# Optimization experiments

Measured on AMD Instinct MI355X. Metric: run time of the kernel, lower is better.

Reference implementation:

```python
import jax, jax.numpy as jnp
import numpy as np

B, T, H, N = 2, 1024, 32, 64
HN = H * N              # 2048 hidden size
KVH, KVD = 8, 512       # GQA kv heads / kv width; repeat = HN // KVD = 4
LW, LA, LV, LG, LK = 64, 64, 32, 128, 32   # wavgk_split_list
EPS = 1e-6

def _rms(x, w):
    xf = x.astype(jnp.float32)
    var = jnp.mean(xf * xf, axis=-1, keepdims=True)
    return (w * (xf * jax.lax.rsqrt(var + EPS))).astype(x.dtype)

def _rot_half(x):
    x1, x2 = jnp.split(x, 2, axis=-1)
    return jnp.concatenate([-x2, x1], axis=-1)

def setup_inputs():
    key = jax.random.key(0)
    ks = iter(jax.random.split(key, 32))
    nrm = lambda s, sc=1.0: jax.random.normal(next(ks), s, jnp.float32) * sc
    d = {
        'x_in': nrm((B, T, HN)),
        'v_first': nrm((B, T, KVH, N)),
        'k_first': nrm((B, T, KVH, N)),
        'state': jnp.zeros((B, H, N, N), jnp.float32),
    }
    pos = jnp.arange(T, dtype=jnp.float32)
    inv = 1.0 / (10000.0 ** (jnp.arange(0, N, 2, dtype=jnp.float32) / N))
    ang = pos[:, None] * inv[None, :]
    ang = jnp.concatenate([ang, ang], axis=-1)   # [T, N]
    d['calc_cos'] = jnp.broadcast_to(jnp.cos(ang), (B, T, N))
    d['calc_sin'] = jnp.broadcast_to(jnp.sin(ang), (B, T, N))
    d.update(
        wavgk1=nrm((HN, LW + LA + LV + LG + LK), 0.02),
        w0=jnp.zeros((HN,), jnp.float32), w2=nrm((LW, HN), 0.02),
        a0=jnp.zeros((HN,), jnp.float32), a2=nrm((LA, HN), 0.02),
        v0=jnp.zeros((KVD,), jnp.float32), v2=nrm((LV, KVD), 0.02),
        g2=nrm((LG, HN), 0.02),
        k0=jnp.zeros((KVD,), jnp.float32), k2=nrm((LK, KVD), 0.02),
        r_k=nrm((H, N), 0.1),
        RKV_w=nrm((HN + 2 * KVD, HN), 0.02),
        O_w=nrm((HN, HN), 0.02),
        R_bias=jnp.zeros((HN,), jnp.float32),
        K_bias=jnp.zeros((KVD,), jnp.float32),
        V_bias=jnp.zeros((KVD,), jnp.float32),
        O_bias=jnp.zeros((HN,), jnp.float32),
        ln_r=jnp.ones((N,), jnp.float32),
        ln_k=jnp.ones((N,), jnp.float32),
        ln1=jnp.ones((HN,), jnp.float32),
    )
    return d

def reference(x_in, v_first, k_first, state, calc_cos, calc_sin, wavgk1, w0, w2,
              a0, a2, v0, v2, g2, k0, k2, r_k, RKV_w, O_w, R_bias, K_bias,
              V_bias, O_bias, ln_r, ln_k, ln1):
    rep = HN // KVD
    x = _rms(x_in, ln1)
    rkv = x @ RKV_w.T                                   # dense form of fpx_matmul
    r, k, v = jnp.split(rkv, [HN, HN + KVD], axis=-1)
    xw, xa, xv, xg, xk = jnp.split(x @ wavgk1, [LW, LW + LA, LW + LA + LV, LW + LA + LV + LG], axis=-1)
    r = r + R_bias; k = k + K_bias; v = v + V_bias
    r = _rms(r.reshape(B, T, H, N), ln_r)
    k = _rms(k.reshape(B, T, KVH, N), ln_k)
    cos, sin = calc_cos[:, :, None, :], calc_sin[:, :, None, :]   # unsqueeze_dim=2
    r = r * cos + _rot_half(r) * sin
    k = k * cos + _rot_half(k) * sin
    v = v.reshape(B, T, KVH, N)
    # layer_id > 0 path: gated residual toward layer-0 v/k
    gate_v = jax.nn.sigmoid(xv @ v2 + v0).reshape(B, T, KVH, N)
    v = v + (v_first - v) * gate_v
    gate_k = jax.nn.sigmoid(xk @ k2 + k0).reshape(B, T, KVH, N)
    k = k + (k_first - k) * gate_k
    w = jnp.tanh(xw) @ w2 + w0
    w = -jax.nn.softplus(-w) - 0.5
    # GQA repeat kv heads to H
    k = jnp.broadcast_to(k[:, :, :, None, :], (B, T, KVH, rep, N)).reshape(B, T, HN)
    v = jnp.broadcast_to(v[:, :, :, None, :], (B, T, KVH, rep, N)).reshape(B, T, HN)
    r = r.reshape(B, T, HN)
    a = jax.nn.sigmoid(xa @ a2 + a0)
    g = jax.nn.sigmoid(xg) @ g2
    kh = k.reshape(B, T, H, N)
    kk = (kh / jnp.maximum(jnp.linalg.norm(kh, axis=-1, keepdims=True), 1e-12)).reshape(B, T, HN)
    k = k * (1.0 - w + a)
    aa, bb = -kk, kk * a
    w = -jnp.exp(w.astype(jnp.float32))                 # log-decay (negative)
    # RWKV-7 recurrence: S <- S*diag(exp(w)) + (S a) b^T + v k^T ; o = S r
    hv = lambda t: jnp.moveaxis(t.reshape(B, T, H, N).astype(jnp.float32), 1, 0)
    def step(S, ts):
        r_t, w_t, k_t, v_t, a_t, b_t = ts               # each [B,H,N]
        sa = jnp.einsum('bhvk,bhk->bhv', S, a_t)
        S = S * jnp.exp(w_t)[:, :, None, :] + sa[..., None] * b_t[:, :, None, :] + v_t[..., None] * k_t[:, :, None, :]
        return S, jnp.einsum('bhvk,bhk->bhv', S, r_t)
    _, o = jax.lax.scan(step, state.astype(jnp.float32), (hv(r), hv(w), hv(k), hv(v), hv(aa), hv(bb)))
    xx = jnp.moveaxis(o, 0, 1).reshape(B, T, HN) * float(N) ** -0.5
    r_, k_, v_ = (t.reshape(B, T, H, N) for t in (r, k, v))
    bonus = (jnp.sum(r_ * k_ * r_k, axis=-1, keepdims=True) * v_).reshape(B, T, HN)
    xx = xx.astype(x_in.dtype) + bonus
    return x_in + (xx * g) @ O_w.T + O_bias
```

## Files before the change

kernel.cpp:

```cpp
#include <hip/hip_runtime.h>
#include <hip/hip_bf16.h>

#define B_ 2
#define T_ 1024
#define H_ 32
#define N_ 64
#define HN_ 2048
#define KVH_ 8
#define KVD_ 512
#define MTOK 2048
#define SMN 7168
#define KCAT 320
#define CH 64
#define NCH 16
#define NCHUNK 1024

typedef __bf16 bf16x8 __attribute__((ext_vector_type(8)));
typedef float f32x4 __attribute__((ext_vector_type(4)));

__device__ __forceinline__ float sigmf(float x) { return 1.f / (1.f + expf(-x)); }

#define PREP_N1 (3072 * 2048)
#define PREP_N2 (2048 * 2048)
#define PREP_N3 (320 * 2048)
#define PREP_N4 (SMN * KCAT)
__global__ void prep_kernel(const float* __restrict__ RKV_w, const float* __restrict__ O_w,
                            const float* __restrict__ wavgk1,
                            const float* __restrict__ w2, const float* __restrict__ a2,
                            const float* __restrict__ v2, const float* __restrict__ g2,
                            const float* __restrict__ k2,
                            __hip_bfloat16* __restrict__ RKVb, __hip_bfloat16* __restrict__ OWb,
                            __hip_bfloat16* __restrict__ WT1b, __hip_bfloat16* __restrict__ Wcatb) {
    long i = (long)blockIdx.x * 256 + threadIdx.x;
    if (i < PREP_N1) { RKVb[i] = __float2bfloat16(RKV_w[i]); return; }
    i -= PREP_N1;
    if (i < PREP_N2) { OWb[i] = __float2bfloat16(O_w[i]); return; }
    i -= PREP_N2;
    if (i < PREP_N3) {
        int c = (int)(i / 2048), r = (int)(i % 2048);
        WT1b[i] = __float2bfloat16(wavgk1[(size_t)r * 320 + c]);
        return;
    }
    i -= PREP_N3;
    if (i >= PREP_N4) return;
    int j = (int)(i / KCAT), k = (int)(i % KCAT);
    float v = 0.f;
    if (j < 2048)      { if (k < 64)             v = w2[(size_t)k * 2048 + j]; }
    else if (j < 4096) { if (k >= 64 && k < 128)  v = a2[(size_t)(k - 64) * 2048 + (j - 2048)]; }
    else if (j < 4608) { if (k >= 128 && k < 160) v = v2[(size_t)(k - 128) * 512 + (j - 4096)]; }
    else if (j < 6656) { if (k >= 160 && k < 288) v = g2[(size_t)(k - 160) * 2048 + (j - 4608)]; }
    else               { if (k >= 288)            v = k2[(size_t)(k - 288) * 512 + (j - 6656)]; }
    Wcatb[i] = __float2bfloat16(v);
}

__global__ __launch_bounds__(256) void rmsnorm_kernel(const float* __restrict__ x,
                                                      const float* __restrict__ ln1,
                                                      __hip_bfloat16* __restrict__ out) {
    const int bt = blockIdx.x, tid = threadIdx.x;
    const float* row = x + (size_t)bt * HN_;
    float4 v0 = *(const float4*)(row + tid * 8);
    float4 v1 = *(const float4*)(row + tid * 8 + 4);
    float s = v0.x*v0.x + v0.y*v0.y + v0.z*v0.z + v0.w*v0.w
            + v1.x*v1.x + v1.y*v1.y + v1.z*v1.z + v1.w*v1.w;
    for (int m = 1; m < 64; m <<= 1) s += __shfl_xor(s, m);
    __shared__ float red[4];
    if ((tid & 63) == 0) red[tid >> 6] = s;
    __syncthreads();
    s = red[0] + red[1] + red[2] + red[3];
    float scale = rsqrtf(s * (1.f / HN_) + 1e-6f);
    float vals[8] = {v0.x, v0.y, v0.z, v0.w, v1.x, v1.y, v1.z, v1.w};
    #pragma unroll
    for (int j = 0; j < 8; ++j)
        out[(size_t)bt * HN_ + tid * 8 + j] = __float2bfloat16(vals[j] * scale * ln1[tid * 8 + j]);
}

__global__ __launch_bounds__(256) void gemm_xw(const __hip_bfloat16* __restrict__ A,
                                               const __hip_bfloat16* __restrict__ B,
                                               __hip_bfloat16* __restrict__ Cb, int M, int N, int K) {
    __shared__ __align__(16) __hip_bfloat16 As[64][40];
    __shared__ __align__(16) __hip_bfloat16 Bs[64][40];
    const int tid = threadIdx.x;
    const int wave = tid >> 6, lane = tid & 63;
    const int wr = (wave >> 1) * 32, wc = (wave & 1) * 32;
    const int brow = blockIdx.y << 6, bcol = blockIdx.x << 6;
    const int lrow = tid >> 2, lcol = (tid & 3) << 3;
    const int fr = lane & 15, ko = (lane >> 4) << 3;
    f32x4 acc[2][2] = {};
    for (int k0 = 0; k0 < K; k0 += 32) {
        uint4 av = *(const uint4*)(A + (size_t)(brow + lrow) * K + k0 + lcol);
        uint4 bv = *(const uint4*)(B + (size_t)(bcol + lrow) * K + k0 + lcol);
        *(uint4*)(&As[lrow][lcol]) = av;
        *(uint4*)(&Bs[lrow][lcol]) = bv;
        __syncthreads();
        bf16x8 af0 = *(const bf16x8*)(&As[wr + fr][ko]);
        bf16x8 af1 = *(const bf16x8*)(&As[wr + 16 + fr][ko]);
        bf16x8 bf0 = *(const bf16x8*)(&Bs[wc + fr][ko]);
        bf16x8 bf1 = *(const bf16x8*)(&Bs[wc + 16 + fr][ko]);
        acc[0][0] = __builtin_amdgcn_mfma_f32_16x16x32_bf16(af0, bf0, acc[0][0], 0, 0, 0);
        acc[0][1] = __builtin_amdgcn_mfma_f32_16x16x32_bf16(af0, bf1, acc[0][1], 0, 0, 0);
        acc[1][0] = __builtin_amdgcn_mfma_f32_16x16x32_bf16(af1, bf0, acc[1][0], 0, 0, 0);
        acc[1][1] = __builtin_amdgcn_mfma_f32_16x16x32_bf16(af1, bf1, acc[1][1], 0, 0, 0);
        __syncthreads();
    }
    const int cr = (lane >> 4) << 2, cc = lane & 15;
    #pragma unroll
    for (int i = 0; i < 2; ++i)
        #pragma unroll
        for (int j = 0; j < 2; ++j)
            #pragma unroll
            for (int r = 0; r < 4; ++r) {
                int row = brow + wr + i * 16 + cr + r;
                int col = bcol + wc + j * 16 + cc;
                float v = acc[i][j][r];
                if (col < 64) v = tanhf(v);
                else if (col >= 160 && col < 288) v = sigmf(v);
                Cb[(size_t)row * N + col] = __float2bfloat16(v);
            }
}

__global__ __launch_bounds__(256) void gemm_bt128(const __hip_bfloat16* __restrict__ A,
                                                  const __hip_bfloat16* __restrict__ B,
                                                  float* __restrict__ C, int M, int N, int K,
                                                  const float* __restrict__ bias,
                                                  const float* __restrict__ addend) {
    __shared__ __align__(16) __hip_bfloat16 As[128][40];
    __shared__ __align__(16) __hip_bfloat16 Bs[128][40];
    const int tid = threadIdx.x;
    const int wave = tid >> 6, lane = tid & 63;
    const int wr = (wave >> 1) * 64, wc = (wave & 1) * 64;
    const int brow = blockIdx.y << 7, bcol = blockIdx.x << 7;
    const int lrow = tid >> 2, lcol = (tid & 3) << 3;
    const int fr = lane & 15, ko = (lane >> 4) << 3;
    f32x4 acc[4][4] = {};
    const __hip_bfloat16* Ap = A + (size_t)(brow + lrow) * K + lcol;
    const __hip_bfloat16* Bp = B + (size_t)(bcol + lrow) * K + lcol;
    const size_t half = (size_t)64 * K;
    for (int k0 = 0; k0 < K; k0 += 32) {
        uint4 a0 = *(const uint4*)(Ap + k0);
        uint4 a1 = *(const uint4*)(Ap + half + k0);
        uint4 b0 = *(const uint4*)(Bp + k0);
        uint4 b1 = *(const uint4*)(Bp + half + k0);
        *(uint4*)(&As[lrow][lcol]) = a0;
        *(uint4*)(&As[lrow + 64][lcol]) = a1;
        *(uint4*)(&Bs[lrow][lcol]) = b0;
        *(uint4*)(&Bs[lrow + 64][lcol]) = b1;
        __syncthreads();
        bf16x8 af[4], bfr[4];
        #pragma unroll
        for (int i = 0; i < 4; ++i) {
            af[i]  = *(const bf16x8*)(&As[wr + i * 16 + fr][ko]);
            bfr[i] = *(const bf16x8*)(&Bs[wc + i * 16 + fr][ko]);
        }
        #pragma unroll
        for (int i = 0; i < 4; ++i)
            #pragma unroll
            for (int j = 0; j < 4; ++j)
                acc[i][j] = __builtin_amdgcn_mfma_f32_16x16x32_bf16(af[i], bfr[j], acc[i][j], 0, 0, 0);
        __syncthreads();
    }
    const int cr = (lane >> 4) << 2, cc = lane & 15;
    #pragma unroll
    for (int i = 0; i < 4; ++i)
        #pragma unroll
        for (int j = 0; j < 4; ++j) {
            const int row0 = brow + wr + i * 16 + cr;
            const int col = bcol + wc + j * 16 + cc;
            #pragma unroll
            for (int r = 0; r < 4; ++r) {
                float v = acc[i][j][r];
                if (bias) v += bias[col];
                if (addend) v += addend[(size_t)(row0 + r) * N + col];
                C[(size_t)(row0 + r) * N + col] = v;
            }
        }
}

__global__ __launch_bounds__(256) void compose_kernel(
    const float* __restrict__ RKV, const float* __restrict__ SM,
    const float* __restrict__ v_first, const float* __restrict__ k_first,
    const float* __restrict__ cosd, const float* __restrict__ sind,
    const float* __restrict__ R_bias, const float* __restrict__ K_bias,
    const float* __restrict__ V_bias, const float* __restrict__ w0,
    const float* __restrict__ a0, const float* __restrict__ v0b,
    const float* __restrict__ k0b, const float* __restrict__ ln_r,
    const float* __restrict__ ln_k, const float* __restrict__ r_k,
    char* __restrict__ SC, __hip_bfloat16* __restrict__ VB, float* __restrict__ SB,
    __hip_bfloat16* __restrict__ G) {
    __shared__ __align__(16) float rbuf[HN_];
    __shared__ __align__(16) float kbuf[KVD_];
    __shared__ __align__(16) float vbuf[KVD_];
    __shared__ float knorms[KVH_];
    __shared__ float cosb[64], sinb[64];
    const int bt = blockIdx.x;
    const int b = bt >> 10, t = bt & 1023;
    const int tid = threadIdx.x;
    const float* rkvrow = RKV + (size_t)bt * 3072;
    const float* smrow = SM + (size_t)bt * SMN;

    if (tid < 64) {
        cosb[tid] = cosd[(size_t)bt * 64 + tid];
        sinb[tid] = sind[(size_t)bt * 64 + tid];
    }

    const int h = tid >> 3;
    const int off = (tid & 7) << 3;
    const int n0 = tid << 3;
    float rraw[8];
    {
        float4 x0 = *(const float4*)(rkvrow + n0);
        float4 x1 = *(const float4*)(rkvrow + n0 + 4);
        float4 b0 = *(const float4*)(R_bias + n0);
        float4 b1 = *(const float4*)(R_bias + n0 + 4);
        rraw[0] = x0.x + b0.x; rraw[1] = x0.y + b0.y; rraw[2] = x0.z + b0.z; rraw[3] = x0.w + b0.w;
        rraw[4] = x1.x + b1.x; rraw[5] = x1.y + b1.y; rraw[6] = x1.z + b1.z; rraw[7] = x1.w + b1.w;
    }
    float rss = 0.f;
    #pragma unroll
    for (int j = 0; j < 8; ++j) { rss += rraw[j] * rraw[j]; rbuf[n0 + j] = rraw[j]; }
    rss += __shfl_xor(rss, 1); rss += __shfl_xor(rss, 2); rss += __shfl_xor(rss, 4);
    float rscale = rsqrtf(rss * (1.f / 64.f) + 1e-6f);

    const int kvh = tid >> 5;
    const int ko2 = (tid & 31) << 1;
    const int kidx = kvh * 64 + ko2;
    float kraw0 = rkvrow[2048 + kidx] + K_bias[kidx];
    float kraw1 = rkvrow[2048 + kidx + 1] + K_bias[kidx + 1];
    float kss = kraw0 * kraw0 + kraw1 * kraw1;
    kss += __shfl_xor(kss, 1); kss += __shfl_xor(kss, 2); kss += __shfl_xor(kss, 4);
    kss += __shfl_xor(kss, 8); kss += __shfl_xor(kss, 16);
    float kscale = rsqrtf(kss * (1.f / 64.f) + 1e-6f);
    kbuf[kidx] = kraw0; kbuf[kidx + 1] = kraw1;

    {
        float va = rkvrow[2560 + kidx] + V_bias[kidx];
        float vb2 = rkvrow[2560 + kidx + 1] + V_bias[kidx + 1];
        float gv0 = sigmf(smrow[4096 + kidx] + v0b[kidx]);
        float gv1 = sigmf(smrow[4096 + kidx + 1] + v0b[kidx + 1]);
        vbuf[kidx] = va + (v_first[(size_t)bt * 512 + kidx] - va) * gv0;
        vbuf[kidx + 1] = vb2 + (v_first[(size_t)bt * 512 + kidx + 1] - vb2) * gv1;
    }
    __syncthreads();

    float rf[8];
    #pragma unroll
    for (int j = 0; j < 8; ++j) {
        int nn = off + j;
        int nn2 = (nn + 32) & 63;
        float val = rbuf[h * 64 + nn] * rscale * ln_r[nn];
        float oth = rbuf[h * 64 + nn2] * rscale * ln_r[nn2];
        float rot = (nn < 32) ? -oth : oth;
        rf[j] = val * cosb[nn] + rot * sinb[nn];
    }
    float kfv[2];
    #pragma unroll
    for (int j = 0; j < 2; ++j) {
        int nn = ko2 + j;
        int nn2 = (nn + 32) & 63;
        float val = kbuf[kvh * 64 + nn] * kscale * ln_k[nn];
        float oth = kbuf[kvh * 64 + nn2] * kscale * ln_k[nn2];
        float rot = (nn < 32) ? -oth : oth;
        float kr = val * cosb[nn] + rot * sinb[nn];
        float gk = sigmf(smrow[6656 + kvh * 64 + nn] + k0b[kvh * 64 + nn]);
        kfv[j] = kr + (k_first[(size_t)bt * 512 + kvh * 64 + nn] - kr) * gk;
    }
    __syncthreads();
    kbuf[kidx] = kfv[0]; kbuf[kidx + 1] = kfv[1];
    float kn = kfv[0] * kfv[0] + kfv[1] * kfv[1];
    kn += __shfl_xor(kn, 1); kn += __shfl_xor(kn, 2); kn += __shfl_xor(kn, 4);
    kn += __shfl_xor(kn, 8); kn += __shfl_xor(kn, 16);
    if ((tid & 31) == 0) knorms[kvh] = fmaxf(sqrtf(kn), 1e-12f);
    __syncthreads();

    const float knv = knorms[h >> 2];
    char* scb = SC + ((size_t)(b * H_ + h) * T_ + t) * 896;
    __hip_bfloat16* us = (__hip_bfloat16*)scb;
    float* df = (float*)(scb + 640);
    float4 w1a = *(const float4*)(smrow + n0);
    float4 w1b = *(const float4*)(smrow + n0 + 4);
    float4 ara = *(const float4*)(smrow + 2048 + n0);
    float4 arb = *(const float4*)(smrow + 2048 + n0 + 4);
    float4 ga  = *(const float4*)(smrow + 4608 + n0);
    float4 gb  = *(const float4*)(smrow + 4608 + n0 + 4);
    float w1arr[8] = {w1a.x, w1a.y, w1a.z, w1a.w, w1b.x, w1b.y, w1b.z, w1b.w};
    float aarr[8] = {ara.x, ara.y, ara.z, ara.w, arb.x, arb.y, arb.z, arb.w};
    float garr[8] = {ga.x, ga.y, ga.z, ga.w, gb.x, gb.y, gb.z, gb.w};
    float bsum = 0.f;
    #pragma unroll
    for (int j = 0; j < 8; ++j) {
        int nn = off + j, n = n0 + j;
        float w1 = w1arr[j] + w0[n];
        float w2v = -log1pf(expf(-w1)) - 0.5f;
        float av = sigmf(aarr[j] + a0[n]);
        float dec = expf(-expf(w2v));
        float kb = kbuf[(h >> 2) * 64 + nn];
        float vbv = vbuf[(h >> 2) * 64 + nn];
        float kkv = kb / knv;
        float ksc = kb * (1.f - w2v + av);
        us[nn]       = __float2bfloat16(rf[j]);
        us[64 + nn]  = __float2bfloat16(ksc);
        us[128 + nn] = __float2bfloat16(-kkv);
        us[192 + nn] = __float2bfloat16(kkv * av);
        us[256 + nn] = __float2bfloat16(vbv);
        df[nn] = dec;
        VB[(size_t)bt * HN_ + n] = __float2bfloat16(vbv);
        G[(size_t)bt * HN_ + n] = __float2bfloat16(garr[j]);
        bsum += rf[j] * ksc * r_k[h * 64 + nn];
    }
    bsum += __shfl_xor(bsum, 1); bsum += __shfl_xor(bsum, 2); bsum += __shfl_xor(bsum, 4);
    if ((tid & 7) == 0) SB[bt * H_ + h] = bsum;
}

__global__ __launch_bounds__(256) void scan_pass1(
    const char* __restrict__ SC, float* __restrict__ Q, float* __restrict__ O,
    float* __restrict__ Pf, float* __restrict__ Sf) {
    const int chunk = blockIdx.x;
    const int bh = chunk >> 4, c = chunk & 15;
    const int b = bh >> 5, h = bh & 31;
    const int tid = threadIdx.x;
    const int wid = tid >> 6, lane = tid & 63;
    const int cq = lane >> 4;
    const int cb = cq << 4;
    const int row = (wid << 4) + (lane & 15);
    const char* base = SC + ((size_t)bh * T_ + (size_t)c * CH) * 896;
    __shared__ __align__(16) float ld[2][6][64];

    f32x4 P4[4], S4[4];
    #pragma unroll
    for (int j = 0; j < 4; ++j)
        #pragma unroll
        for (int e = 0; e < 4; ++e) {
            P4[j][e] = (cb + 4 * j + e == row) ? 1.f : 0.f;
            S4[j][e] = 0.f;
        }

    float p0 = 0.f, p1 = 0.f;
    auto LOADT = [&](int t) {
        const __hip_bfloat16* us = (const __hip_bfloat16*)(base + (size_t)t * 896);
        if (wid == 0)      { p0 = __bfloat162float(us[128 + lane]); p1 = __bfloat162float(us[lane]); }
        else if (wid == 1) { p0 = __bfloat162float(us[192 + lane]); p1 = __bfloat162float(us[256 + lane]); }
        else if (wid == 2) { p0 = *(const float*)(base + (size_t)t * 896 + 640 + 4 * lane); }
        else               { p0 = __bfloat162float(us[64 + lane]); }
    };
    LOADT(0);
    float* qrow = Q + (size_t)chunk * CH * 64 + row;
    float* orow = O + ((size_t)b * T_ + (size_t)c * CH) * HN_ + h * 64 + row;
    for (int t = 0; t < CH; ++t) {
        const int buf = t & 1;
        if (wid == 0)      { ld[buf][0][lane] = p0; ld[buf][4][lane] = p1; }
        else if (wid == 1) { ld[buf][1][lane] = p0; ld[buf][5][lane] = p1; }
        else if (wid == 2) { ld[buf][2][lane] = p0; }
        else               { ld[buf][3][lane] = p0; }
        __syncthreads();
        if (t + 1 < CH) LOADT(t + 1);
        f32x4 a4[4];
        #pragma unroll
        for (int j = 0; j < 4; ++j) a4[j] = *(const f32x4*)&ld[buf][0][cb + 4 * j];
        f32x4 dpv = {0,0,0,0}, dsv = {0,0,0,0};
        #pragma unroll
        for (int j = 0; j < 4; ++j) { dpv += P4[j] * a4[j]; dsv += S4[j] * a4[j]; }
        float dp = dpv[0] + dpv[1] + dpv[2] + dpv[3];
        float dsd = dsv[0] + dsv[1] + dsv[2] + dsv[3];
        dp += __shfl_xor(dp, 16);  dp += __shfl_xor(dp, 32);
        dsd += __shfl_xor(dsd, 16); dsd += __shfl_xor(dsd, 32);
        const float vt = ld[buf][5][row];
        const f32x4 cPv = {dp, dp, dp, dp}, sav = {dsd, dsd, dsd, dsd}, vtv = {vt, vt, vt, vt};
        f32x4 qp = {0,0,0,0}, op = {0,0,0,0};
        #pragma unroll
        for (int j = 0; j < 4; ++j) {
            f32x4 d4 = *(const f32x4*)&ld[buf][2][cb + 4 * j];
            f32x4 b4 = *(const f32x4*)&ld[buf][1][cb + 4 * j];
            f32x4 k4 = *(const f32x4*)&ld[buf][3][cb + 4 * j];
            f32x4 r4 = *(const f32x4*)&ld[buf][4][cb + 4 * j];
            f32x4 Pn = P4[j] * d4 + cPv * b4;
            f32x4 Sn = S4[j] * d4 + sav * b4 + vtv * k4;
            P4[j] = Pn; S4[j] = Sn;
            qp += Pn * r4; op += Sn * r4;
        }
        float qs = qp[0] + qp[1] + qp[2] + qp[3];
        float os = op[0] + op[1] + op[2] + op[3];
        qs += __shfl_xor(qs, 16); qs += __shfl_xor(qs, 32);
        os += __shfl_xor(os, 16); os += __shfl_xor(os, 32);
        if (cq == 0) {
            qrow[(size_t)t * 64] = qs;
            orow[(size_t)t * HN_] = os;
        }
    }
    float* pf = Pf + (size_t)chunk * 4096 + (size_t)row * 64 + cb;
    float* sf = Sf + (size_t)chunk * 4096 + (size_t)row * 64 + cb;
    #pragma unroll
    for (int j = 0; j < 4; ++j) {
        *(f32x4*)(pf + 4 * j) = P4[j];
        *(f32x4*)(sf + 4 * j) = S4[j];
    }
}

__global__ __launch_bounds__(256) void scan_pass2(
    const float* __restrict__ Pf, float* __restrict__ Sf, const float* __restrict__ state) {
    const int blk = blockIdx.x;
    const int bh = blk >> 2, rb = blk & 3;
    const int tid = threadIdx.x;
    const int lv = tid >> 4, c0 = (tid & 15) << 2;
    __shared__ __align__(16) float S[16][68];
    __shared__ __align__(16) float P[64][64];

    *(f32x4*)&S[lv][c0] = *(const f32x4*)&state[(size_t)bh * 4096 + 1024 * rb + tid * 4];
    const size_t pbase = (size_t)(bh * NCH) * 4096;
    {
        f32x4 p0[4];
        #pragma unroll
        for (int j = 0; j < 4; ++j) p0[j] = *(const f32x4*)&Pf[pbase + tid * 16 + 4 * j];
        #pragma unroll
        for (int j = 0; j < 4; ++j) *(f32x4*)(&P[0][0] + tid * 16 + 4 * j) = p0[j];
    }
    __syncthreads();

    for (int c = 0; c < NCH; ++c) {
        const size_t ck = (size_t)(bh * NCH + c) * 4096;
        f32x4 pp[4];
        if (c + 1 < NCH) {
            #pragma unroll
            for (int j = 0; j < 4; ++j) pp[j] = *(const f32x4*)&Pf[ck + 4096 + tid * 16 + 4 * j];
        }
        f32x4 acc = *(const f32x4*)&Sf[ck + 1024 * rb + tid * 4];
        f32x4 cur = *(const f32x4*)&S[lv][c0];
        #pragma unroll 4
        for (int k4 = 0; k4 < 64; k4 += 4) {
            f32x4 sk4 = *(const f32x4*)&S[lv][k4];
            #pragma unroll
            for (int kk = 0; kk < 4; ++kk) {
                f32x4 pr = *(const f32x4*)&P[k4 + kk][c0];
                f32x4 sv = {sk4[kk], sk4[kk], sk4[kk], sk4[kk]};
                acc += sv * pr;
            }
        }
        __syncthreads();
        *(f32x4*)&S[lv][c0] = acc;
        if (c + 1 < NCH) {
            #pragma unroll
            for (int j = 0; j < 4; ++j) *(f32x4*)(&P[0][0] + tid * 16 + 4 * j) = pp[j];
        }
        *(f32x4*)&Sf[ck + 1024 * rb + tid * 4] = cur;
        __syncthreads();
    }
}

__global__ __launch_bounds__(64) void pass3_post(
    const float* __restrict__ Q, const float* __restrict__ Sinit, const float* __restrict__ OL,
    const float* __restrict__ SB, const __hip_bfloat16* __restrict__ VB,
    const __hip_bfloat16* __restrict__ G, __hip_bfloat16* __restrict__ Ub) {
    const int chunk = blockIdx.x;
    const int bh = chunk >> 4, c = chunk & 15;
    const int b = bh >> 5, h = bh & 31;
    const int t = threadIdx.x;
    __shared__ __align__(16) float S[64][64];
    #pragma unroll
    for (int j = 0; j < 16; ++j)
        *(f32x4*)&S[t][4 * j] = *(const f32x4*)&Sinit[(size_t)chunk * 4096 + (size_t)t * 64 + 4 * j];
    __syncthreads();
    float q[64];
    #pragma unroll
    for (int j = 0; j < 16; ++j)
        *(f32x4*)&q[4 * j] = *(const f32x4*)&Q[((size_t)chunk * CH + t) * 64 + 4 * j];
    const size_t bt = (size_t)b * T_ + (size_t)c * CH + t;
    const float sb = SB[bt * H_ + h];
    const float* olrow = OL + bt * HN_ + h * 64;
    const __hip_bfloat16* vbrow = VB + bt * HN_ + h * 64;
    const __hip_bfloat16* grow = G + bt * HN_ + h * 64;
    __hip_bfloat16* urow = Ub + bt * HN_ + h * 64;
    #pragma unroll 4
    for (int v = 0; v < 64; ++v) {
        f32x4 a = {0, 0, 0, 0};
        #pragma unroll
        for (int j = 0; j < 16; ++j)
            a += *(const f32x4*)&S[v][4 * j] * *(const f32x4*)&q[4 * j];
        float o = (a[0] + a[1] + a[2] + a[3] + olrow[v]) * 0.125f;
        float u = (o + sb * __bfloat162float(vbrow[v])) * __bfloat162float(grow[v]);
        urow[v] = __float2bfloat16(u);
    }
}

extern "C" void kernel_launch(void* const* d_in, const int* in_sizes, int n_in,
                              void* d_out, int out_size, void* d_ws, size_t ws_size,
                              hipStream_t stream) {
    (void)in_sizes; (void)n_in; (void)out_size; (void)ws_size;
    const float* x_in    = (const float*)d_in[0];
    const float* v_first = (const float*)d_in[1];
    const float* k_first = (const float*)d_in[2];
    const float* state   = (const float*)d_in[3];
    const float* calc_cos= (const float*)d_in[4];
    const float* calc_sin= (const float*)d_in[5];
    const float* wavgk1  = (const float*)d_in[6];
    const float* w0      = (const float*)d_in[7];
    const float* w2      = (const float*)d_in[8];
    const float* a0      = (const float*)d_in[9];
    const float* a2      = (const float*)d_in[10];
    const float* v0      = (const float*)d_in[11];
    const float* v2      = (const float*)d_in[12];
    const float* g2      = (const float*)d_in[13];
    const float* k0      = (const float*)d_in[14];
    const float* k2      = (const float*)d_in[15];
    const float* r_k     = (const float*)d_in[16];
    const float* RKV_w   = (const float*)d_in[17];
    const float* O_w     = (const float*)d_in[18];
    const float* R_bias  = (const float*)d_in[19];
    const float* K_bias  = (const float*)d_in[20];
    const float* V_bias  = (const float*)d_in[21];
    const float* O_bias  = (const float*)d_in[22];
    const float* ln_r    = (const float*)d_in[23];
    const float* ln_k    = (const float*)d_in[24];
    const float* ln1     = (const float*)d_in[25];
    float* out = (float*)d_out;

    char* ws = (char*)d_ws;
    size_t off = 0;
    auto alloc = [&](size_t bytes) -> char* {
        char* p = ws + off;
        off = (off + bytes + 255) & ~(size_t)255;
        return p;
    };
    char*  SCb = alloc((size_t)64 * T_ * 896);
    __hip_bfloat16* Ub = (__hip_bfloat16*)SCb;
    __hip_bfloat16* VBb = (__hip_bfloat16*)alloc((size_t)MTOK * HN_ * 2);
    __hip_bfloat16* Gb  = (__hip_bfloat16*)alloc((size_t)MTOK * HN_ * 2);
    float* SBf = (float*)alloc((size_t)MTOK * H_ * 4);
    float* Of  = (float*)alloc((size_t)MTOK * HN_ * 4);
    __hip_bfloat16* OWb = (__hip_bfloat16*)alloc((size_t)2048 * 2048 * 2);

    size_t ovl = off;
    float* SMf = (float*)alloc((size_t)MTOK * SMN * 4);
    __hip_bfloat16* Xb     = (__hip_bfloat16*)alloc((size_t)MTOK * HN_ * 2);
    __hip_bfloat16* RKVb   = (__hip_bfloat16*)alloc((size_t)3072 * 2048 * 2);
    __hip_bfloat16* WT1b   = (__hip_bfloat16*)alloc((size_t)320 * 2048 * 2);
    __hip_bfloat16* Wcatb  = (__hip_bfloat16*)alloc((size_t)SMN * KCAT * 2);
    __hip_bfloat16* XWmodb = (__hip_bfloat16*)alloc((size_t)MTOK * KCAT * 2);
    float* RKVf  = (float*)alloc((size_t)MTOK * 3072 * 4);
    off = ovl;
    float* Qf  = (float*)alloc((size_t)NCHUNK * CH * 64 * 4);
    float* Pff = (float*)alloc((size_t)NCHUNK * 4096 * 4);
    float* Sff = (float*)alloc((size_t)NCHUNK * 4096 * 4);

    {
        long total = (long)PREP_N1 + PREP_N2 + PREP_N3 + PREP_N4;
        prep_kernel<<<(int)((total + 255) / 256), 256, 0, stream>>>(
            RKV_w, O_w, wavgk1, w2, a2, v2, g2, k2, RKVb, OWb, WT1b, Wcatb);
    }

    rmsnorm_kernel<<<MTOK, 256, 0, stream>>>(x_in, ln1, Xb);

    gemm_bt128<<<dim3(3072 / 128, MTOK / 128), 256, 0, stream>>>(Xb, RKVb, RKVf, MTOK, 3072, 2048, nullptr, nullptr);
    gemm_xw<<<dim3(320 / 64, MTOK / 64), 256, 0, stream>>>(Xb, WT1b, XWmodb, MTOK, 320, 2048);
    gemm_bt128<<<dim3(SMN / 128, MTOK / 128), 256, 0, stream>>>(XWmodb, Wcatb, SMf, MTOK, SMN, KCAT, nullptr, nullptr);

    compose_kernel<<<MTOK, 256, 0, stream>>>(RKVf, SMf, v_first, k_first, calc_cos, calc_sin,
                                             R_bias, K_bias, V_bias, w0, a0, v0, k0,
                                             ln_r, ln_k, r_k, SCb, VBb, SBf, Gb);

    scan_pass1<<<NCHUNK, 256, 0, stream>>>(SCb, Qf, Of, Pff, Sff);
    scan_pass2<<<B_ * H_ * 4, 256, 0, stream>>>(Pff, Sff, state);
    pass3_post<<<NCHUNK, 64, 0, stream>>>(Qf, Sff, Of, SBf, VBb, Gb, Ub);

    gemm_bt128<<<dim3(HN_ / 128, MTOK / 128), 256, 0, stream>>>(Ub, OWb, out, MTOK, HN_, 2048, O_bias, x_in);
}
```

Measured before the change: 437.2 us.

## Split-K the low-rank projection GEMM and use direct global-to-LDS loads in main GEMM

The narrow 320-column projection GEMM is split four ways along K into fp32 partial buffers, and a new reduce kernel sums the partials and applies tanh/sigmoid. This gives the small-grid kernel more blocks to fill the GPU. Separately, gemm_bt128 now stages its tiles with global_load_lds (direct global-to-LDS DMA) into unpadded 32-wide LDS rows instead of loading through registers. Dropping the padding may add LDS bank conflicts on the fragment reads, and the split-K adds an extra launch and partial-buffer traffic.

```diff
diff --git a/kernel.cpp b/kernel.cpp
--- a/kernel.cpp
+++ b/kernel.cpp
@@ -1,5 +1,6 @@
 #include <hip/hip_runtime.h>
 #include <hip/hip_bf16.h>
+#include <stdint.h>
 
 #define B_ 2
 #define T_ 1024
@@ -17,6 +18,12 @@
 
 typedef __bf16 bf16x8 __attribute__((ext_vector_type(8)));
 typedef float f32x4 __attribute__((ext_vector_type(4)));
+
+typedef __attribute__((address_space(1))) uint32_t gu32;
+typedef __attribute__((address_space(3))) uint32_t lu32;
+__device__ __forceinline__ void gload16(const void* g, void* l) {
+    __builtin_amdgcn_global_load_lds((gu32*)g, (lu32*)l, 16, 0, 0);
+}
 
 __device__ __forceinline__ float sigmf(float x) { return 1.f / (1.f + expf(-x)); }
 
@@ -74,19 +81,21 @@
         out[(size_t)bt * HN_ + tid * 8 + j] = __float2bfloat16(vals[j] * scale * ln1[tid * 8 + j]);
 }
 
-__global__ __launch_bounds__(256) void gemm_xw(const __hip_bfloat16* __restrict__ A,
-                                               const __hip_bfloat16* __restrict__ B,
-                                               __hip_bfloat16* __restrict__ Cb, int M, int N, int K) {
+__global__ __launch_bounds__(256) void gemm_xw_sk(const __hip_bfloat16* __restrict__ A,
+                                                  const __hip_bfloat16* __restrict__ B,
+                                                  float* __restrict__ Cp, int M, int N, int K) {
     __shared__ __align__(16) __hip_bfloat16 As[64][40];
     __shared__ __align__(16) __hip_bfloat16 Bs[64][40];
     const int tid = threadIdx.x;
     const int wave = tid >> 6, lane = tid & 63;
     const int wr = (wave >> 1) * 32, wc = (wave & 1) * 32;
     const int brow = blockIdx.y << 6, bcol = blockIdx.x << 6;
+    const int z = blockIdx.z;
+    const int kbeg = z * (K >> 2), kend = kbeg + (K >> 2);
     const int lrow = tid >> 2, lcol = (tid & 3) << 3;
     const int fr = lane & 15, ko = (lane >> 4) << 3;
     f32x4 acc[2][2] = {};
-    for (int k0 = 0; k0 < K; k0 += 32) {
+    for (int k0 = kbeg; k0 < kend; k0 += 32) {
         uint4 av = *(const uint4*)(A + (size_t)(brow + lrow) * K + k0 + lcol);
         uint4 bv = *(const uint4*)(B + (size_t)(bcol + lrow) * K + k0 + lcol);
         *(uint4*)(&As[lrow][lcol]) = av;
@@ -103,6 +112,7 @@
         __syncthreads();
     }
     const int cr = (lane >> 4) << 2, cc = lane & 15;
+    float* Cz = Cp + (size_t)z * M * N;
     #pragma unroll
     for (int i = 0; i < 2; ++i)
         #pragma unroll
@@ -111,11 +121,19 @@
             for (int r = 0; r < 4; ++r) {
                 int row = brow + wr + i * 16 + cr + r;
                 int col = bcol + wc + j * 16 + cc;
-                float v = acc[i][j][r];
-                if (col < 64) v = tanhf(v);
-                else if (col >= 160 && col < 288) v = sigmf(v);
-                Cb[(size_t)row * N + col] = __float2bfloat16(v);
+                Cz[(size_t)row * N + col] = acc[i][j][r];
             }
+}
+
+__global__ void xw_reduce(const float* __restrict__ Cp, __hip_bfloat16* __restrict__ out) {
+    long i = (long)blockIdx.x * 256 + threadIdx.x;
+    if (i >= (long)MTOK * KCAT) return;
+    const long MN = (long)MTOK * KCAT;
+    float v = Cp[i] + Cp[i + MN] + Cp[i + 2 * MN] + Cp[i + 3 * MN];
+    int c = (int)(i % KCAT);
+    if (c < 64) v = tanhf(v);
+    else if (c >= 160 && c < 288) v = sigmf(v);
+    out[i] = __float2bfloat16(v);
 }
 
 __global__ __launch_bounds__(256) void gemm_bt128(const __hip_bfloat16* __restrict__ A,
@@ -123,27 +141,26 @@
                                                   float* __restrict__ C, int M, int N, int K,
                                                   const float* __restrict__ bias,
                                                   const float* __restrict__ addend) {
-    __shared__ __align__(16) __hip_bfloat16 As[128][40];
-    __shared__ __align__(16) __hip_bfloat16 Bs[128][40];
+    __shared__ __align__(16) __hip_bfloat16 As[128][32];
+    __shared__ __align__(16) __hip_bfloat16 Bs[128][32];
     const int tid = threadIdx.x;
     const int wave = tid >> 6, lane = tid & 63;
     const int wr = (wave >> 1) * 64, wc = (wave & 1) * 64;
     const int brow = blockIdx.y << 7, bcol = blockIdx.x << 7;
-    const int lrow = tid >> 2, lcol = (tid & 3) << 3;
     const int fr = lane & 15, ko = (lane >> 4) << 3;
+    const int ar0 = wave * 32;
+    const int sr = lane >> 2;
+    const int sc = (lane & 3) << 3;
     f32x4 acc[4][4] = {};
-    const __hip_bfloat16* Ap = A + (size_t)(brow + lrow) * K + lcol;
-    const __hip_bfloat16* Bp = B + (size_t)(bcol + lrow) * K + lcol;
-    const size_t half = (size_t)64 * K;
+    const __hip_bfloat16* gA0 = A + (size_t)(brow + ar0 + sr) * K + sc;
+    const __hip_bfloat16* gA1 = A + (size_t)(brow + ar0 + 16 + sr) * K + sc;
+    const __hip_bfloat16* gB0 = B + (size_t)(bcol + ar0 + sr) * K + sc;
+    const __hip_bfloat16* gB1 = B + (size_t)(bcol + ar0 + 16 + sr) * K + sc;
     for (int k0 = 0; k0 < K; k0 += 32) {
-        uint4 a0 = *(const uint4*)(Ap + k0);
-        uint4 a1 = *(const uint4*)(Ap + half + k0);
-        uint4 b0 = *(const uint4*)(Bp + k0);
-        uint4 b1 = *(const uint4*)(Bp + half + k0);
-        *(uint4*)(&As[lrow][lcol]) = a0;
-        *(uint4*)(&As[lrow + 64][lcol]) = a1;
-        *(uint4*)(&Bs[lrow][lcol]) = b0;
-        *(uint4*)(&Bs[lrow + 64][lcol]) = b1;
+        gload16(gA0 + k0, &As[ar0][0]);
+        gload16(gA1 + k0, &As[ar0 + 16][0]);
+        gload16(gB0 + k0, &Bs[ar0][0]);
+        gload16(gB1 + k0, &Bs[ar0 + 16][0]);
         __syncthreads();
         bf16x8 af[4], bfr[4];
         #pragma unroll
@@ -534,6 +551,7 @@
     __hip_bfloat16* Wcatb  = (__hip_bfloat16*)alloc((size_t)SMN * KCAT * 2);
     __hip_bfloat16* XWmodb = (__hip_bfloat16*)alloc((size_t)MTOK * KCAT * 2);
     float* RKVf  = (float*)alloc((size_t)MTOK * 3072 * 4);
+    float* XWp   = (float*)alloc((size_t)4 * MTOK * KCAT * 4);
     off = ovl;
     float* Qf  = (float*)alloc((size_t)NCHUNK * CH * 64 * 4);
     float* Pff = (float*)alloc((size_t)NCHUNK * 4096 * 4);
@@ -548,7 +566,8 @@
     rmsnorm_kernel<<<MTOK, 256, 0, stream>>>(x_in, ln1, Xb);
 
     gemm_bt128<<<dim3(3072 / 128, MTOK / 128), 256, 0, stream>>>(Xb, RKVb, RKVf, MTOK, 3072, 2048, nullptr, nullptr);
-    gemm_xw<<<dim3(320 / 64, MTOK / 64), 256, 0, stream>>>(Xb, WT1b, XWmodb, MTOK, 320, 2048);
+    gemm_xw_sk<<<dim3(KCAT / 64, MTOK / 64, 4), 256, 0, stream>>>(Xb, WT1b, XWp, MTOK, KCAT, 2048);
+    xw_reduce<<<(MTOK * KCAT + 255) / 256, 256, 0, stream>>>(XWp, XWmodb);
     gemm_bt128<<<dim3(SMN / 128, MTOK / 128), 256, 0, stream>>>(XWmodb, Wcatb, SMf, MTOK, SMN, KCAT, nullptr, nullptr);
 
     compose_kernel<<<MTOK, 256, 0, stream>>>(RKVf, SMf, v_first, k_first, calc_cos, calc_sin,
```

Result: faster. 420.7 us (-3.8%).
